# Optimization experiments

Measured on AMD Instinct MI355X. Metric: run time of the kernel, lower is better.

Reference implementation:

```python
import jax, jax.numpy as jnp
import numpy as np

EPS = 1e-8
SMOOTH = 9.0
N_IMAGE, N_REGIONS, N_CAP, MAX_WORDS = 64, 36, 64, 40
EMBED, SIM_DIM = 1024, 256


def l2norm(x, axis=-1):
    n = jnp.sqrt(jnp.sum(x * x, axis=axis, keepdims=True)) + EPS
    return x / n


def setup_inputs() -> dict:
    key = jax.random.key(0)
    k1, k2, k3, k4 = jax.random.split(key, 4)
    img_emb = jax.random.normal(k1, (N_IMAGE, N_REGIONS, EMBED), dtype=jnp.float32)
    cap_emb = jax.random.normal(k2, (N_CAP, MAX_WORDS, EMBED), dtype=jnp.float32)
    cap_lens = jax.random.randint(k3, (N_CAP,), 10, MAX_WORDS + 1)
    # zero out padded words so the batched formulation matches the per-caption loop
    mask = (jnp.arange(MAX_WORDS)[None, :] < cap_lens[:, None]).astype(jnp.float32)
    cap_emb = cap_emb * mask[:, :, None]
    adjs = jnp.zeros((N_CAP, MAX_WORDS, MAX_WORDS), dtype=jnp.int32)
    depends = jnp.zeros((N_CAP, MAX_WORDS, MAX_WORDS), dtype=jnp.int32)
    r = np.sqrt(6.0) / np.sqrt(EMBED + SIM_DIM)
    W = jax.random.uniform(k4, (EMBED, SIM_DIM), minval=-r, maxval=r, dtype=jnp.float32)
    b = jnp.zeros((SIM_DIM,), dtype=jnp.float32)
    return {"img_emb": img_emb, "cap_emb": cap_emb, "cap_lens": cap_lens,
            "adjs": adjs, "depends": depends, "W": W, "b": b}


def reference(img_emb, cap_emb, cap_lens, adjs, depends, W, b):
    C, L, D = cap_emb.shape
    mask = (jnp.arange(L)[None, :] < cap_lens[:, None]).astype(cap_emb.dtype)  # (C, L)
    cap = cap_emb * mask[:, :, None]
    # attn: (C, I, R, L) = context . query^T for every (caption, image) pair
    attn = jnp.einsum('ird,cld->cirl', img_emb, cap)
    attn = jax.nn.leaky_relu(attn, negative_slope=0.1)
    # l2norm over the word dim (padded words contribute exactly 0)
    attn = attn / (jnp.sqrt(jnp.sum(attn * attn, axis=3, keepdims=True)) + EPS)
    # softmax over regions after transpose + smooth scaling: (C, I, L, R)
    attn = jax.nn.softmax(jnp.swapaxes(attn, 2, 3) * SMOOTH, axis=3)
    wc = jnp.einsum('cilr,ird->cild', attn, img_emb)  # (C, I, L, D)
    wc = l2norm(wc, axis=-1)
    sim = jnp.square(wc - cap[:, None, :, :])
    out = l2norm(jax.nn.relu(sim @ W + b), axis=-1)
    # zero padded-word rows (the original returns only :n_word slices)
    out = out * mask[:, None, :, None]
    return out  # (C, I, L, SIM_DIM)
```

## Files before the change

### kernel.cpp

```cpp
#include <hip/hip_runtime.h>

#define C_N 64
#define I_N 64
#define R_N 36
#define L_N 40
#define D_N 1024
#define S_N 256

#define P_LD 72

#define OFF_CAP 2359296
#define OFF_WT  4980736
#define OFF_IMT 5242880
#define OFF_SLK 8388608
#define OFF_SIM 8388672
#define M_ALL   (C_N * I_N * L_N)
#define CH_STRIDE ((size_t)M_ALL * 32)
#define OFF_G   (OFF_SIM + 32 * CH_STRIDE)
#define OFF_P   (OFF_G + I_N * 48 * 64)

typedef float f4 __attribute__((ext_vector_type(4)));
typedef short s16x8 __attribute__((ext_vector_type(8)));
typedef short s16x4 __attribute__((ext_vector_type(4)));

__device__ __forceinline__ unsigned short f2bs(float f) {
    union { float f; unsigned u; } v; v.f = f;
    unsigned r = v.u + 0x7FFFu + ((v.u >> 16) & 1u);
    return (unsigned short)(r >> 16);
}
__device__ __forceinline__ float bs2f(unsigned short s) {
    union { unsigned u; float f; } v; v.u = ((unsigned)s) << 16;
    return v.f;
}
__device__ __forceinline__ void async16(const unsigned short* g, unsigned short* l) {
    __builtin_amdgcn_global_load_lds(
        (const __attribute__((address_space(1))) unsigned int*)g,
        (__attribute__((address_space(3))) unsigned int*)l, 16, 0, 0);
}

__global__ void k_convert(const float* __restrict__ img, const float* __restrict__ cap,
                          const float* __restrict__ W, unsigned short* __restrict__ ws) {
    int t = blockIdx.x * 256 + threadIdx.x;
    if (t < I_N * R_N * D_N) ws[t] = f2bs(img[t]);
    if (t < C_N * L_N * D_N) ws[OFF_CAP + t] = f2bs(cap[t]);
    if (t < D_N * S_N) {
        int d = t >> 8, s = t & 255;
        int ch = d >> 5, wi = d & 31;
        int md = wi >> 4, r = wi & 15, q = r >> 2, j = r & 3;
        int ep = q * 8 + md * 4 + j;
        ws[OFF_WT + ((ch * 256 + s) * 32) + ep] = f2bs(W[t]);
    }
    if (t < 64) ws[OFF_SLK + t] = 0;
}

__global__ void k_scan(const int* __restrict__ lens, int* __restrict__ P) {
    if (threadIdx.x == 0) {
        int a = 0;
        for (int c = 0; c < C_N; ++c) { P[c] = a; a += lens[c]; }
        P[C_N] = a;
    }
}

__global__ __launch_bounds__(256)
void k_zero(const int* __restrict__ lens, float* __restrict__ out) {
    int idx = blockIdx.x * 256 + threadIdx.x;
    int row = idx >> 6, sq = (idx & 63) << 2;
    int c = row / (I_N * L_N);
    int l = row % L_N;
    if (l >= lens[c]) {
        f4 z = {};
        __builtin_nontemporal_store(z, (f4*)(out + (size_t)row * S_N + sq));
    }
}

__global__ __launch_bounds__(256)
void k_imt(const float* __restrict__ img, unsigned short* __restrict__ imt) {
    __shared__ unsigned short t[64][50];
    const int i = blockIdx.y, d0 = blockIdx.x * 64;
    const int tid = threadIdx.x;
    #pragma unroll
    for (int it = 0; it < 9; ++it) {
        int e = it * 256 + tid;
        int r = e >> 6, dc = e & 63;
        t[dc][r] = f2bs(img[((size_t)i * R_N + r) * D_N + d0 + dc]);
    }
    #pragma unroll
    for (int it = 0; it < 3; ++it) {
        int e = it * 256 + tid;
        t[e & 63][36 + (e >> 6)] = 0;
    }
    __syncthreads();
    #pragma unroll
    for (int it = 0; it < 6; ++it) {
        int e = it * 256 + tid;
        int dc = e / 24, wd = e - dc * 24;
        unsigned v = (unsigned)t[dc][2 * wd] | ((unsigned)t[dc][2 * wd + 1] << 16);
        ((unsigned*)imt)[(size_t)(i * D_N + d0 + dc) * 24 + wd] = v;
    }
}

__global__ __launch_bounds__(64)
void k_gram(const unsigned short* __restrict__ img_b, unsigned short* __restrict__ g) {
    const int i = blockIdx.x;
    const int lane = threadIdx.x;
    const int q = lane >> 4, ln16 = lane & 15;
    const unsigned short* ai = img_b + i * (R_N * D_N);
    unsigned short* gi = g + i * (48 * 64);
    for (int e = lane; e < 48 * 8; e += 64) {
        int r = e >> 3, wd = e & 7;
        ((unsigned*)(gi + r * 64 + 48))[wd] = 0;
    }
    f4 c[3][3] = {};
    #pragma unroll 4
    for (int ks = 0; ks < 32; ++ks) {
        const int kb = ks * 32 + q * 8;
        s16x8 af[3];
        af[0] = *(const s16x8*)(ai + ln16 * D_N + kb);
        af[1] = *(const s16x8*)(ai + (16 + ln16) * D_N + kb);
        af[2] = (ln16 < 4) ? *(const s16x8*)(ai + (32 + ln16) * D_N + kb) : (s16x8)0;
        #pragma unroll
        for (int mt = 0; mt < 3; ++mt)
            #pragma unroll
            for (int nt = 0; nt < 3; ++nt)
                c[mt][nt] = __builtin_amdgcn_mfma_f32_16x16x32_bf16(af[mt], af[nt], c[mt][nt], 0, 0, 0);
    }
    #pragma unroll
    for (int mt = 0; mt < 3; ++mt)
        #pragma unroll
        for (int nt = 0; nt < 3; ++nt)
            #pragma unroll
            for (int j = 0; j < 4; ++j)
                gi[(mt * 16 + q * 4 + j) * 64 + nt * 16 + ln16] = f2bs(c[mt][nt][j]);
}

__global__ __launch_bounds__(512, 4)
void k_pre(const unsigned short* __restrict__ img_b,
           const unsigned short* __restrict__ cap_b,
           const unsigned short* __restrict__ img_t,
           const unsigned short* __restrict__ gram,
           const int* __restrict__ lens,
           const int* __restrict__ P,
           unsigned short* __restrict__ simg) {
    __shared__ __align__(16) unsigned short s_p[8][48 * P_LD];

    const int n = blockIdx.y * 8 + blockIdx.x;
    const int x = n & 7, m = n >> 3;
    const int i   = ((x & 3) << 4) | (m >> 2);
    const int oct = ((x >> 2) << 2) | (m & 3);
    const int wave = threadIdx.x >> 6, lane = threadIdx.x & 63;
    const int c = oct * 8 + wave;
    const int q = lane >> 4, ln16 = lane & 15;

    const int len = lens[c];
    const int NL = (len > 32) ? 3 : (len > 16 ? 2 : 1);
    const int rowbase = P[c] * 64 + i * len;

    const unsigned short* ai = img_b + i * (R_N * D_N);
    const unsigned short* bc = cap_b + c * (L_N * D_N);
    const unsigned short* imtc = img_t + (size_t)i * D_N * 48;
    unsigned short* sp = &s_p[wave][0];

    for (int k = lane; k < 48 * P_LD / 2; k += 64) ((unsigned*)sp)[k] = 0;

    f4 acc[3][3] = {};
    #pragma unroll 4
    for (int ks = 0; ks < 32; ++ks) {
        const int kb = ks * 32 + q * 8;
        s16x8 af[3], bf[3];
        af[0] = *(const s16x8*)(ai + ln16 * D_N + kb);
        af[1] = *(const s16x8*)(ai + (16 + ln16) * D_N + kb);
        af[2] = (ln16 < 4) ? *(const s16x8*)(ai + (32 + ln16) * D_N + kb) : (s16x8)0;
        bf[0] = *(const s16x8*)(bc + ln16 * D_N + kb);
        bf[1] = (NL > 1) ? *(const s16x8*)(bc + (16 + ln16) * D_N + kb) : (s16x8)0;
        bf[2] = (NL > 2 && ln16 < 8) ? *(const s16x8*)(bc + (32 + ln16) * D_N + kb) : (s16x8)0;
        #pragma unroll
        for (int mt = 0; mt < 3; ++mt)
            #pragma unroll
            for (int nt = 0; nt < 3; ++nt)
                if (nt < NL)
                    acc[mt][nt] = __builtin_amdgcn_mfma_f32_16x16x32_bf16(af[mt], bf[nt], acc[mt][nt], 0, 0, 0);
    }

    #pragma unroll
    for (int mt = 0; mt < 3; ++mt)
        #pragma unroll
        for (int nt = 0; nt < 3; ++nt)
            #pragma unroll
            for (int j = 0; j < 4; ++j) {
                float v = acc[mt][nt][j];
                acc[mt][nt][j] = (v > 0.f) ? v : 0.1f * v;
            }
    #pragma unroll
    for (int mt = 0; mt < 3; ++mt)
        #pragma unroll
        for (int j = 0; j < 4; ++j) {
            float ss = 0.f;
            #pragma unroll
            for (int nt = 0; nt < 3; ++nt) ss += acc[mt][nt][j] * acc[mt][nt][j];
            #pragma unroll
            for (int o = 1; o < 16; o <<= 1) ss += __shfl_xor(ss, o, 64);
            float inv = 1.f / (sqrtf(ss) + 1e-8f);
            #pragma unroll
            for (int nt = 0; nt < 3; ++nt) acc[mt][nt][j] *= inv;
        }
    #pragma unroll
    for (int nt = 0; nt < 3; ++nt) {
        if (nt < NL) {
            const int l = nt * 16 + ln16;
            float mx = -1e30f;
            #pragma unroll
            for (int mt = 0; mt < 3; ++mt)
                #pragma unroll
                for (int j = 0; j < 4; ++j) {
                    int r = mt * 16 + q * 4 + j;
                    if (r < R_N) mx = fmaxf(mx, 9.f * acc[mt][nt][j]);
                }
            mx = fmaxf(mx, __shfl_xor(mx, 16, 64));
            mx = fmaxf(mx, __shfl_xor(mx, 32, 64));
            float sum = 0.f;
            #pragma unroll
            for (int mt = 0; mt < 3; ++mt)
                #pragma unroll
                for (int j = 0; j < 4; ++j) {
                    int r = mt * 16 + q * 4 + j;
                    float e = (r < R_N) ? __expf(9.f * acc[mt][nt][j] - mx) : 0.f;
                    acc[mt][nt][j] = e;
                    sum += e;
                }
            sum += __shfl_xor(sum, 16, 64);
            sum += __shfl_xor(sum, 32, 64);
            float inv = 1.f / sum;
            #pragma unroll
            for (int mt = 0; mt < 3; ++mt)
                #pragma unroll
                for (int j = 0; j < 4; ++j) {
                    int r = mt * 16 + q * 4 + j;
                    if (r < R_N && l < L_N) sp[l * P_LD + r] = f2bs(acc[mt][nt][j] * inv);
                }
        }
    }

    s16x8 paf[3][2];
    #pragma unroll
    for (int nl = 0; nl < 3; ++nl)
        #pragma unroll
        for (int ks = 0; ks < 2; ++ks)
            paf[nl][ks] = *(const s16x8*)(sp + (nl * 16 + ln16) * P_LD + ks * 32 + q * 8);

    const unsigned short* gi = gram + i * (48 * 64);
    f4 T[3][3] = {};
    #pragma unroll
    for (int ks = 0; ks < 2; ++ks) {
        const int kb = ks * 32 + q * 8;
        s16x8 ga[3];
        #pragma unroll
        for (int mt = 0; mt < 3; ++mt)
            ga[mt] = *(const s16x8*)(gi + (mt * 16 + ln16) * 64 + kb);
        #pragma unroll
        for (int mt = 0; mt < 3; ++mt)
            #pragma unroll
            for (int nl = 0; nl < 3; ++nl)
                if (nl < NL)
                    T[mt][nl] = __builtin_amdgcn_mfma_f32_16x16x32_bf16(ga[mt], paf[nl][ks], T[mt][nl], 0, 0, 0);
    }
    float inv2[3] = {0.f, 0.f, 0.f};
    #pragma unroll
    for (int nl = 0; nl < 3; ++nl) {
        if (nl < NL) {
            const int l = nl * 16 + ln16;
            float rsl = 0.f;
            #pragma unroll
            for (int mt = 0; mt < 3; ++mt) {
                const s16x4 pv = *(const s16x4*)(sp + l * P_LD + mt * 16 + q * 4);
                #pragma unroll
                for (int j = 0; j < 4; ++j)
                    rsl += bs2f((unsigned short)pv[j]) * T[mt][nl][j];
            }
            rsl += __shfl_xor(rsl, 16, 64);
            rsl += __shfl_xor(rsl, 32, 64);
            inv2[nl] = 1.f / (sqrtf(rsl) + 1e-8f);
        }
    }

    #pragma unroll 2
    for (int ch = 0; ch < 32; ++ch) {
        f4 a2[2][3] = {};
        #pragma unroll
        for (int ks = 0; ks < 2; ++ks) {
            const int kb = ks * 32 + q * 8;
            #pragma unroll
            for (int md = 0; md < 2; ++md) {
                const int drow = ch * 32 + md * 16 + ln16;
                s16x8 afr = *(const s16x8*)(imtc + drow * 48 + kb);
                #pragma unroll
                for (int nl = 0; nl < 3; ++nl)
                    if (nl < NL)
                        a2[md][nl] = __builtin_amdgcn_mfma_f32_16x16x32_bf16(afr, paf[nl][ks], a2[md][nl], 0, 0, 0);
            }
        }
        const size_t chbase = (size_t)ch * CH_STRIDE + (size_t)rowbase * 32;
        #pragma unroll
        for (int nl = 0; nl < 3; ++nl) {
            if (nl < NL) {
                const int l = nl * 16 + ln16;
                if (l < len) {
                    const float iv = inv2[nl];
                    s16x8 ov;
                    #pragma unroll
                    for (int md = 0; md < 2; ++md) {
                        const int db = ch * 32 + md * 16 + q * 4;
                        const s16x4 cv = *(const s16x4*)(bc + l * D_N + db);
                        #pragma unroll
                        for (int j = 0; j < 4; ++j) {
                            float dv = a2[md][nl][j] * iv - bs2f((unsigned short)cv[j]);
                            ov[md * 4 + j] = (short)f2bs(dv * dv);
                        }
                    }
                    __builtin_nontemporal_store(ov,
                        (s16x8*)(simg + chbase + (size_t)l * 32 + q * 8));
                }
            }
        }
    }
}

__global__ __launch_bounds__(512, 4)
void k_gemm3(const unsigned short* __restrict__ simt,
             const unsigned short* __restrict__ wtt,
             const int* __restrict__ P,
             const float* __restrict__ bias,
             float* __restrict__ out) {
    __shared__ __align__(16) unsigned short sA[2][128 * 32];
    __shared__ __align__(16) unsigned short sB[2][256 * 32];
    __shared__ float s_sum[128];

    const int m0 = blockIdx.x * 128;
    const int Mv = P[C_N] * 64;
    if (m0 >= Mv) return;

    const int tid = threadIdx.x;
    const int w = tid >> 6, lane = tid & 63;
    const int ln16 = lane & 15, q = lane >> 4;
    const int wm = (w >> 2) * 64, wn = (w & 3) * 64;
    const int srow = tid >> 2;
    const int swz = ((tid & 3) ^ ((srow >> 1) & 3)) << 3;
    const unsigned short* gA  = simt + ((size_t)(m0 + srow)) * 32 + swz;
    const unsigned short* gB0 = wtt + (size_t)srow * 32 + swz;
    const unsigned short* gB1 = wtt + (size_t)(128 + srow) * 32 + swz;
    unsigned short* const lA = (unsigned short*)sA + tid * 8;
    unsigned short* const lB = (unsigned short*)sB + tid * 8;

    if (tid < 128) s_sum[tid] = 0.f;

    async16(gA + (size_t)31 * CH_STRIDE, lA);
    async16(gB0 + 31 * 8192, lB);
    async16(gB1 + 31 * 8192, lB + 4096);

    f4 acc[4][4] = {};
    #pragma unroll 1
    for (int t = 0; t < 31; ++t) {
        const int nb = (t + 1) & 1;
        const int pch = 30 - t;
        async16(gA + (size_t)pch * CH_STRIDE, lA + nb * 4096);
        async16(gB0 + pch * 8192, lB + nb * 8192);
        async16(gB1 + pch * 8192, lB + nb * 8192 + 4096);
        asm volatile("s_waitcnt vmcnt(3)" ::: "memory");
        __builtin_amdgcn_s_barrier();
        __builtin_amdgcn_sched_barrier(0);
        const unsigned short* cA = (const unsigned short*)sA + (t & 1) * 4096;
        const unsigned short* cB = (const unsigned short*)sB + (t & 1) * 8192;
        s16x8 af[4], bf[4];
        #pragma unroll
        for (int mt = 0; mt < 4; ++mt) {
            int row = wm + mt * 16 + ln16;
            af[mt] = *(const s16x8*)(cA + row * 32 + ((q ^ ((row >> 1) & 3)) << 3));
        }
        #pragma unroll
        for (int nt = 0; nt < 4; ++nt) {
            int row = wn + nt * 16 + ln16;
            bf[nt] = *(const s16x8*)(cB + row * 32 + ((q ^ ((row >> 1) & 3)) << 3));
        }
        #pragma unroll
        for (int mt = 0; mt < 4; ++mt)
            #pragma unroll
            for (int nt = 0; nt < 4; ++nt)
                acc[mt][nt] = __builtin_amdgcn_mfma_f32_16x16x32_bf16(af[mt], bf[nt], acc[mt][nt], 0, 0, 0);
        __builtin_amdgcn_s_barrier();
    }
    asm volatile("s_waitcnt vmcnt(0)" ::: "memory");
    __builtin_amdgcn_s_barrier();
    __builtin_amdgcn_sched_barrier(0);
    {
        const unsigned short* cA = (const unsigned short*)sA + 4096;
        const unsigned short* cB = (const unsigned short*)sB + 8192;
        s16x8 af[4], bf[4];
        #pragma unroll
        for (int mt = 0; mt < 4; ++mt) {
            int row = wm + mt * 16 + ln16;
            af[mt] = *(const s16x8*)(cA + row * 32 + ((q ^ ((row >> 1) & 3)) << 3));
        }
        #pragma unroll
        for (int nt = 0; nt < 4; ++nt) {
            int row = wn + nt * 16 + ln16;
            bf[nt] = *(const s16x8*)(cB + row * 32 + ((q ^ ((row >> 1) & 3)) << 3));
        }
        #pragma unroll
        for (int mt = 0; mt < 4; ++mt)
            #pragma unroll
            for (int nt = 0; nt < 4; ++nt)
                acc[mt][nt] = __builtin_amdgcn_mfma_f32_16x16x32_bf16(af[mt], bf[nt], acc[mt][nt], 0, 0, 0);
    }

    float bv[4];
    #pragma unroll
    for (int nt = 0; nt < 4; ++nt) bv[nt] = bias[wn + nt * 16 + ln16];
    #pragma unroll
    for (int mt = 0; mt < 4; ++mt)
        #pragma unroll
        for (int j = 0; j < 4; ++j) {
            float s = 0.f;
            #pragma unroll
            for (int nt = 0; nt < 4; ++nt) {
                float v = acc[mt][nt][j] + bv[nt];
                v = fmaxf(v, 0.f);
                acc[mt][nt][j] = v;
                s += v * v;
            }
            #pragma unroll
            for (int o = 1; o < 16; o <<= 1) s += __shfl_xor(s, o, 64);
            if (ln16 == 0) atomicAdd(&s_sum[wm + mt * 16 + q * 4 + j], s);
        }
    __syncthreads();
    if (tid < 128) {
        int grow = m0 + tid;
        s_sum[tid] = (grow < Mv) ? 1.f / (sqrtf(s_sum[tid]) + 1e-8f) : 0.f;
    }
    __syncthreads();
    #pragma unroll
    for (int mt = 0; mt < 4; ++mt)
        #pragma unroll
        for (int j = 0; j < 4; ++j) {
            const int rt = wm + mt * 16 + q * 4 + j;
            const int grow = m0 + rt;
            if (grow < Mv) {
                int lo = 0, hi = C_N;
                while (hi - lo > 1) {
                    int mid = (lo + hi) >> 1;
                    if (P[mid] * 64 <= grow) lo = mid; else hi = mid;
                }
                const int lenc = P[lo + 1] - P[lo];
                const int rem = grow - P[lo] * 64;
                const int ii = rem / lenc;
                const int ll = rem - ii * lenc;
                const float sc = s_sum[rt];
                float* op = out + (size_t)((lo * I_N + ii) * L_N + ll) * S_N + wn;
                #pragma unroll
                for (int nt = 0; nt < 4; ++nt)
                    __builtin_nontemporal_store(acc[mt][nt][j] * sc,
                        op + nt * 16 + ln16);
            }
        }
}

extern "C" void kernel_launch(void* const* d_in, const int* in_sizes, int n_in,
                              void* d_out, int out_size, void* d_ws, size_t ws_size,
                              hipStream_t stream) {
    const float* img  = (const float*)d_in[0];
    const float* cap  = (const float*)d_in[1];
    const int*   lens = (const int*)d_in[2];
    const float* W    = (const float*)d_in[5];
    const float* bias = (const float*)d_in[6];
    float* out = (float*)d_out;
    unsigned short* ws = (unsigned short*)d_ws;
    int* P = (int*)(ws + OFF_P);

    k_convert<<<10240, 256, 0, stream>>>(img, cap, W, ws);
    k_scan<<<1, 64, 0, stream>>>(lens, P);
    k_zero<<<M_ALL / 4, 256, 0, stream>>>(lens, out);
    dim3 gridT(16, I_N);
    k_imt<<<gridT, 256, 0, stream>>>(img, ws + OFF_IMT);
    k_gram<<<I_N, 64, 0, stream>>>(ws, ws + OFF_G);

    dim3 gridP(8, I_N);
    k_pre<<<gridP, 512, 0, stream>>>(ws, ws + OFF_CAP, ws + OFF_IMT, ws + OFF_G,
                                     lens, P, ws + OFF_SIM);

    k_gemm3<<<M_ALL / 128, 512, 0, stream>>>(ws + OFF_SIM, ws + OFF_WT, P, bias, out);
}
```

Before: 477.0 us.

## Fold scan and padded-row zeroing into other kernels, split gram K across waves

```diff
diff --git a/kernel.cpp b/kernel.cpp
--- a/kernel.cpp
+++ b/kernel.cpp
@@ -39,7 +39,8 @@
 }
 
 __global__ void k_convert(const float* __restrict__ img, const float* __restrict__ cap,
-                          const float* __restrict__ W, unsigned short* __restrict__ ws) {
+                          const float* __restrict__ W, unsigned short* __restrict__ ws,
+                          const int* __restrict__ lens, int* __restrict__ P) {
     int t = blockIdx.x * 256 + threadIdx.x;
     if (t < I_N * R_N * D_N) ws[t] = f2bs(img[t]);
     if (t < C_N * L_N * D_N) ws[OFF_CAP + t] = f2bs(cap[t]);
@@ -51,25 +52,16 @@
         ws[OFF_WT + ((ch * 256 + s) * 32) + ep] = f2bs(W[t]);
     }
     if (t < 64) ws[OFF_SLK + t] = 0;
-}
-
-__global__ void k_scan(const int* __restrict__ lens, int* __restrict__ P) {
-    if (threadIdx.x == 0) {
-        int a = 0;
-        for (int c = 0; c < C_N; ++c) { P[c] = a; a += lens[c]; }
-        P[C_N] = a;
-    }
-}
-
-__global__ __launch_bounds__(256)
-void k_zero(const int* __restrict__ lens, float* __restrict__ out) {
-    int idx = blockIdx.x * 256 + threadIdx.x;
-    int row = idx >> 6, sq = (idx & 63) << 2;
-    int c = row / (I_N * L_N);
-    int l = row % L_N;
-    if (l >= lens[c]) {
-        f4 z = {};
-        __builtin_nontemporal_store(z, (f4*)(out + (size_t)row * S_N + sq));
+    if (blockIdx.x == 0 && threadIdx.x < 64) {
+        int lane = threadIdx.x;
+        int v = lens[lane];
+        #pragma unroll
+        for (int o = 1; o < 64; o <<= 1) {
+            int u = __shfl_up(v, o, 64);
+            if (lane >= o) v += u;
+        }
+        P[lane + 1] = v;
+        if (lane == 0) P[0] = 0;
     }
 }
 
@@ -99,21 +91,23 @@
     }
 }
 
-__global__ __launch_bounds__(64)
+__global__ __launch_bounds__(256)
 void k_gram(const unsigned short* __restrict__ img_b, unsigned short* __restrict__ g) {
+    __shared__ float sg[3][64][36];
     const int i = blockIdx.x;
-    const int lane = threadIdx.x;
+    const int wv = threadIdx.x >> 6, lane = threadIdx.x & 63;
     const int q = lane >> 4, ln16 = lane & 15;
     const unsigned short* ai = img_b + i * (R_N * D_N);
     unsigned short* gi = g + i * (48 * 64);
-    for (int e = lane; e < 48 * 8; e += 64) {
-        int r = e >> 3, wd = e & 7;
-        ((unsigned*)(gi + r * 64 + 48))[wd] = 0;
-    }
+    if (wv == 3)
+        for (int e = lane; e < 48 * 8; e += 64) {
+            int r = e >> 3, wd = e & 7;
+            ((unsigned*)(gi + r * 64 + 48))[wd] = 0;
+        }
     f4 c[3][3] = {};
-    #pragma unroll 4
-    for (int ks = 0; ks < 32; ++ks) {
-        const int kb = ks * 32 + q * 8;
+    #pragma unroll
+    for (int kk = 0; kk < 8; ++kk) {
+        const int kb = (wv * 8 + kk) * 32 + q * 8;
         s16x8 af[3];
         af[0] = *(const s16x8*)(ai + ln16 * D_N + kb);
         af[1] = *(const s16x8*)(ai + (16 + ln16) * D_N + kb);
@@ -124,13 +118,28 @@
             for (int nt = 0; nt < 3; ++nt)
                 c[mt][nt] = __builtin_amdgcn_mfma_f32_16x16x32_bf16(af[mt], af[nt], c[mt][nt], 0, 0, 0);
     }
-    #pragma unroll
-    for (int mt = 0; mt < 3; ++mt)
-        #pragma unroll
-        for (int nt = 0; nt < 3; ++nt)
-            #pragma unroll
-            for (int j = 0; j < 4; ++j)
-                gi[(mt * 16 + q * 4 + j) * 64 + nt * 16 + ln16] = f2bs(c[mt][nt][j]);
+    if (wv) {
+        #pragma unroll
+        for (int mt = 0; mt < 3; ++mt)
+            #pragma unroll
+            for (int nt = 0; nt < 3; ++nt)
+                #pragma unroll
+                for (int j = 0; j < 4; ++j)
+                    sg[wv - 1][lane][(mt * 3 + nt) * 4 + j] = c[mt][nt][j];
+    }
+    __syncthreads();
+    if (wv == 0) {
+        #pragma unroll
+        for (int mt = 0; mt < 3; ++mt)
+            #pragma unroll
+            for (int nt = 0; nt < 3; ++nt)
+                #pragma unroll
+                for (int j = 0; j < 4; ++j) {
+                    const int idx = (mt * 3 + nt) * 4 + j;
+                    float s = c[mt][nt][j] + sg[0][lane][idx] + sg[1][lane][idx] + sg[2][lane][idx];
+                    gi[(mt * 16 + q * 4 + j) * 64 + nt * 16 + ln16] = f2bs(s);
+                }
+    }
 }
 
 __global__ __launch_bounds__(512, 4)
@@ -316,8 +325,7 @@
                             ov[md * 4 + j] = (short)f2bs(dv * dv);
                         }
                     }
-                    __builtin_nontemporal_store(ov,
-                        (s16x8*)(simg + chbase + (size_t)l * 32 + q * 8));
+                    *(s16x8*)(simg + chbase + (size_t)l * 32 + q * 8) = ov;
                 }
             }
         }
@@ -336,7 +344,22 @@
 
     const int m0 = blockIdx.x * 128;
     const int Mv = P[C_N] * 64;
-    if (m0 >= Mv) return;
+    if (m0 >= Mv) {
+        const int nAct = (Mv + 127) >> 7;
+        const int E = gridDim.x - nAct;
+        const int z = blockIdx.x - nAct;
+        const int r0 = (int)((long)M_ALL * z / E);
+        const int r1 = (int)((long)M_ALL * (z + 1) / E);
+        const int lane = threadIdx.x & 63, wv = threadIdx.x >> 6;
+        f4 zz = {};
+        for (int row = r0 + wv; row < r1; row += 8) {
+            const int cc = row / (I_N * L_N);
+            const int ll = row % L_N;
+            if (ll >= P[cc + 1] - P[cc])
+                __builtin_nontemporal_store(zz, (f4*)(out + (size_t)row * S_N + lane * 4));
+        }
+        return;
+    }
 
     const int tid = threadIdx.x;
     const int w = tid >> 6, lane = tid & 63;
@@ -474,12 +497,10 @@
     unsigned short* ws = (unsigned short*)d_ws;
     int* P = (int*)(ws + OFF_P);
 
-    k_convert<<<10240, 256, 0, stream>>>(img, cap, W, ws);
-    k_scan<<<1, 64, 0, stream>>>(lens, P);
-    k_zero<<<M_ALL / 4, 256, 0, stream>>>(lens, out);
+    k_convert<<<10240, 256, 0, stream>>>(img, cap, W, ws, lens, P);
     dim3 gridT(16, I_N);
     k_imt<<<gridT, 256, 0, stream>>>(img, ws + OFF_IMT);
-    k_gram<<<I_N, 64, 0, stream>>>(ws, ws + OFF_G);
+    k_gram<<<I_N, 256, 0, stream>>>(ws, ws + OFF_G);
 
     dim3 gridP(8, I_N);
     k_pre<<<gridP, 512, 0, stream>>>(ws, ws + OFF_CAP, ws + OFF_IMT, ws + OFF_G,
```

Result: faster. 457.8 us (-4.0%).
